# Kernel tuning notes

Hardware: AMD Instinct MI355X
Metric: run time of the kernel (lower is better)

## Reference

```python
import jax, jax.numpy as jnp
import numpy as np

EMBED = 512
HEADS = 8
HEAD_DIM = EMBED // HEADS
N, T = 512, 64


def setup_inputs() -> dict:
    key = jax.random.key(0)
    ks = jax.random.split(key, 11)
    s = 1.0 / np.sqrt(EMBED)
    inp = {
        'values': jax.random.normal(ks[0], (N, T, EMBED), jnp.float32),
        'keys':   jax.random.normal(ks[1], (N, T, EMBED), jnp.float32),
        'query':  jax.random.normal(ks[2], (N, T, EMBED), jnp.float32),
        'Wv': jax.random.uniform(ks[3], (EMBED, EMBED), jnp.float32, -s, s),
        'bv': jax.random.uniform(ks[4], (EMBED,), jnp.float32, -s, s),
        'Wk': jax.random.uniform(ks[5], (EMBED, EMBED), jnp.float32, -s, s),
        'bk': jax.random.uniform(ks[6], (EMBED,), jnp.float32, -s, s),
        'Wq': jax.random.uniform(ks[7], (EMBED, EMBED), jnp.float32, -s, s),
        'bq': jax.random.uniform(ks[8], (EMBED,), jnp.float32, -s, s),
        'Wo': jax.random.uniform(ks[9], (EMBED, EMBED), jnp.float32, -s, s),
        'bo': jax.random.uniform(ks[10], (EMBED,), jnp.float32, -s, s),
    }
    return inp


def reference(values, keys, query, Wv, bv, Wk, bk, Wq, bq, Wo, bo):
    n, t, c = query.shape
    v = (values @ Wv.T + bv).reshape(n, t, HEADS, HEAD_DIM)
    k = (keys   @ Wk.T + bk).reshape(n, t, HEADS, HEAD_DIM)
    q = (query  @ Wq.T + bq).reshape(n, t, HEADS, HEAD_DIM)
    # attention over the batch axis: energy[q,k,t,h]
    energy = jnp.einsum('qthd,kthd->qkth', q, k)
    attn = jax.nn.softmax(energy / jnp.sqrt(jnp.float32(EMBED)), axis=1)
    out = jnp.einsum('qkth,kthd->qthd', attn, v).reshape(n, t, HEADS * HEAD_DIM)
    return out @ Wo.T + bo
```

## Files before the change

kernel.cpp:

```cpp
#include <hip/hip_runtime.h>
#include <hip/hip_bf16.h>
#include <math.h>

#define NBATCH 512
#define TT 64
#define EMB 512
#define NHEADS 8
#define HDIM 64
#define MROWS (NBATCH * TT)
#define ROWSTRIDE (TT * EMB)
#define WSEG 262144

static constexpr float QSCALE = 0.0637587140f;

typedef __attribute__((ext_vector_type(8))) short short8v;
typedef __attribute__((ext_vector_type(4))) float f32x4;

__device__ __forceinline__ unsigned short f2bf(float x) {
    union { float f; unsigned int u; } v; v.f = x;
    unsigned int r = v.u + 0x7fff + ((v.u >> 16) & 1);
    return (unsigned short)(r >> 16);
}

__device__ __forceinline__ unsigned int cvtpk(float lo, float hi) {
    unsigned int r;
    asm("v_cvt_pk_bf16_f32 %0, %1, %2" : "=v"(r) : "v"(lo), "v"(hi));
    return r;
}

__device__ __forceinline__ void gl16(const void* g, void* l) {
    __builtin_amdgcn_global_load_lds(
        (const __attribute__((address_space(1))) unsigned int*)g,
        (__attribute__((address_space(3))) unsigned int*)l, 16, 0, 0);
}

__global__ __launch_bounds__(256) void cvt3(
    const float* __restrict__ a, const float* __restrict__ b, const float* __restrict__ c,
    unsigned short* __restrict__ oa, unsigned short* __restrict__ ob, unsigned short* __restrict__ oc)
{
    const size_t i = (size_t)blockIdx.x * 256 + threadIdx.x;
    float4 va = reinterpret_cast<const float4*>(a)[i];
    float4 vb = reinterpret_cast<const float4*>(b)[i];
    float4 vc = reinterpret_cast<const float4*>(c)[i];
    ushort4 ra, rb, rc;
    ra.x = f2bf(va.x); ra.y = f2bf(va.y); ra.z = f2bf(va.z); ra.w = f2bf(va.w);
    rb.x = f2bf(vb.x); rb.y = f2bf(vb.y); rb.z = f2bf(vb.z); rb.w = f2bf(vb.w);
    rc.x = f2bf(vc.x); rc.y = f2bf(vc.y); rc.z = f2bf(vc.z); rc.w = f2bf(vc.w);
    reinterpret_cast<ushort4*>(oa)[i] = ra;
    reinterpret_cast<ushort4*>(ob)[i] = rb;
    reinterpret_cast<ushort4*>(oc)[i] = rc;
}

__global__ __launch_bounds__(256) void cvtw(
    const float* __restrict__ w0, const float* __restrict__ w1,
    const float* __restrict__ w2, const float* __restrict__ w3,
    unsigned short* __restrict__ dst)
{
    const int seg = blockIdx.y;
    const float* src = (seg == 0) ? w0 : (seg == 1) ? w1 : (seg == 2) ? w2 : w3;
    const float sc = (seg == 0) ? QSCALE : 1.0f;
    const size_t i = (size_t)blockIdx.x * 256 + threadIdx.x;
    float4 v = reinterpret_cast<const float4*>(src)[i];
    ushort4 r;
    r.x = f2bf(v.x * sc); r.y = f2bf(v.y * sc); r.z = f2bf(v.z * sc); r.w = f2bf(v.w * sc);
    reinterpret_cast<ushort4*>(dst + (size_t)seg * WSEG)[i] = r;
}

__global__ __launch_bounds__(512, 2) void gemm_proj3(
    const unsigned short* __restrict__ A0, const unsigned short* __restrict__ A1,
    const unsigned short* __restrict__ A2, const unsigned short* __restrict__ Wb,
    const float* __restrict__ b0, const float* __restrict__ b1, const float* __restrict__ b2,
    unsigned short* __restrict__ o0, unsigned short* __restrict__ o1, unsigned short* __restrict__ o2)
{
    __shared__ __align__(16) unsigned short Asb[2][256 * 64];
    __shared__ __align__(16) unsigned short Bsb[2][256 * 64];
    const int z = blockIdx.z;
    const unsigned short* A = (z == 0) ? A0 : (z == 1) ? A1 : A2;
    const unsigned short* W = Wb + (size_t)z * WSEG;
    const float* bias = (z == 0) ? b0 : (z == 1) ? b1 : b2;
    const float bsc = (z == 0) ? QSCALE : 1.0f;
    unsigned short* Cout = (z == 0) ? o0 : (z == 1) ? o1 : o2;

    const int tid = threadIdx.x;
    const int wave = tid >> 6, lane = tid & 63;
    const int lg = lane >> 4, li = lane & 15;
    const int m0 = blockIdx.x * 256;
    const int n0 = blockIdx.y * 256;
    const int wm = (wave >> 2) * 128;
    const int wn = (wave & 3) * 64;

    f32x4 acc[8][4] = {};

    const int au = (tid & 7) ^ ((tid >> 3) & 7);
    const unsigned short* gA = A + (size_t)(m0 + (tid >> 3)) * 512 + au * 8;
    const unsigned short* gW = W + (size_t)(n0 + (tid >> 3)) * 512 + au * 8;

#define ISSUE(t, bb) do {                                                   \
        const int _k0 = (t) * 64;                                           \
        _Pragma("unroll")                                                   \
        for (int _i = 0; _i < 4; _i++) {                                    \
            gl16(gA + _k0 + (size_t)_i * 64 * 512,                          \
                 &Asb[bb][wave * 512 + _i * 4096]);                         \
            gl16(gW + _k0 + (size_t)_i * 64 * 512,                          \
                 &Bsb[bb][wave * 512 + _i * 4096]);                         \
        }                                                                   \
    } while (0)

    ISSUE(0, 0);
    ISSUE(1, 1);

    for (int t = 0; t < 8; ++t) {
        if (t < 7) { asm volatile("s_waitcnt vmcnt(8)" ::: "memory"); }
        else       { asm volatile("s_waitcnt vmcnt(0)" ::: "memory"); }
        __builtin_amdgcn_s_barrier();
        __builtin_amdgcn_sched_barrier(0);

        const int b = t & 1;
        __builtin_amdgcn_s_setprio(1);
#pragma unroll
        for (int kf = 0; kf < 2; kf++) {
            const int xofs = (kf * 32 + lg * 8);
            short8v bfr[4];
#pragma unroll
            for (int nf = 0; nf < 4; nf++) {
                const int rB = wn + nf * 16 + li;
                bfr[nf] = *reinterpret_cast<const short8v*>(
                    &Bsb[b][rB * 64 + (xofs ^ ((rB & 7) * 8))]);
            }
#pragma unroll
            for (int mf = 0; mf < 8; mf++) {
                const int rA = wm + mf * 16 + li;
                const short8v af = *reinterpret_cast<const short8v*>(
                    &Asb[b][rA * 64 + (xofs ^ ((rA & 7) * 8))]);
#pragma unroll
                for (int nf = 0; nf < 4; nf++)
                    acc[mf][nf] = __builtin_amdgcn_mfma_f32_16x16x32_bf16(af, bfr[nf], acc[mf][nf], 0, 0, 0);
            }
        }
        __builtin_amdgcn_s_setprio(0);

        asm volatile("s_waitcnt lgkmcnt(0)" ::: "memory");
        __builtin_amdgcn_s_barrier();
        __builtin_amdgcn_sched_barrier(0);
        if (t + 2 < 8) ISSUE(t + 2, b);
    }
#undef ISSUE

#pragma unroll
    for (int nf = 0; nf < 4; nf++) {
        const int col = n0 + wn + nf * 16 + li;
        const float bb = bias[col] * bsc;
#pragma unroll
        for (int mf = 0; mf < 8; mf++) {
            const int row0 = m0 + wm + mf * 16 + lg * 4;
#pragma unroll
            for (int r = 0; r < 4; r++)
                Cout[(size_t)(row0 + r) * 512 + col] = f2bf(acc[mf][nf][r] + bb);
        }
    }
}

__global__ __launch_bounds__(256) void gemm_out(
    const unsigned short* __restrict__ A, const unsigned short* __restrict__ W,
    const float* __restrict__ bias, float* __restrict__ Cout)
{
    __shared__ __align__(16) unsigned short As[128 * 32];
    __shared__ __align__(16) unsigned short Bs[128 * 32];
    const int tid = threadIdx.x;
    const int wave = tid >> 6, lane = tid & 63;
    const int lg = lane >> 4, li = lane & 15;
    const int m0 = blockIdx.x * 128;
    const int n0 = blockIdx.y * 128;
    const int wr = (wave >> 1) * 64;
    const int wc = (wave & 1) * 64;

    f32x4 acc[4][4] = {};

    const unsigned short* ga = A + (size_t)(m0 + (tid >> 2)) * 512 + (tid & 3) * 8;
    const unsigned short* gb = W + (size_t)(n0 + (tid >> 2)) * 512 + (tid & 3) * 8;
    unsigned short* lA = &As[wave * 512];
    unsigned short* lB = &Bs[wave * 512];

    for (int k0 = 0; k0 < 512; k0 += 32) {
        __syncthreads();
        gl16(ga + k0, lA);
        gl16(ga + k0 + 64 * 512, lA + 2048);
        gl16(gb + k0, lB);
        gl16(gb + k0 + 64 * 512, lB + 2048);
        __syncthreads();

        short8v af[4], bfr[4];
#pragma unroll
        for (int i = 0; i < 4; i++) {
            af[i]  = *reinterpret_cast<const short8v*>(&As[(wr + i * 16 + li) * 32 + lg * 8]);
            bfr[i] = *reinterpret_cast<const short8v*>(&Bs[(wc + i * 16 + li) * 32 + lg * 8]);
        }
#pragma unroll
        for (int i = 0; i < 4; i++)
#pragma unroll
            for (int j = 0; j < 4; j++)
                acc[i][j] = __builtin_amdgcn_mfma_f32_16x16x32_bf16(af[i], bfr[j], acc[i][j], 0, 0, 0);
    }

#pragma unroll
    for (int j = 0; j < 4; j++) {
        const int col = n0 + wc + j * 16 + li;
        const float bb = bias[col];
#pragma unroll
        for (int i = 0; i < 4; i++) {
            const int row0 = m0 + wr + i * 16 + lg * 4;
#pragma unroll
            for (int r = 0; r < 4; r++)
                Cout[(size_t)(row0 + r) * 512 + col] = acc[i][j][r] + bb;
        }
    }
}

__global__ __launch_bounds__(256) void attn_bf16(
    const unsigned short* __restrict__ qp, const unsigned short* __restrict__ kp,
    const unsigned short* __restrict__ vp, unsigned short* __restrict__ ao)
{
    __shared__ __align__(16) unsigned short Ks[64 * 64];
    __shared__ __align__(16) unsigned short Vt[64][68];
    __shared__ __align__(16) unsigned short Pl[4][16][72];

    const int tid = threadIdx.x;
    const int wave = tid >> 6, lane = tid & 63;
    const int lg = lane >> 4, li = lane & 15;
    const int n0 = blockIdx.x * 256;
    const int th = blockIdx.y;
    const size_t base = (size_t)(th >> 3) * EMB + (size_t)(th & 7) * HDIM;

    short8v qf[4][2];
#pragma unroll
    for (int mf = 0; mf < 4; mf++)
#pragma unroll
        for (int kf = 0; kf < 2; kf++)
            qf[mf][kf] = *reinterpret_cast<const short8v*>(
                qp + (size_t)(n0 + wave * 64 + mf * 16 + li) * ROWSTRIDE
                   + base + kf * 32 + lg * 8);

    const int vd0 = (tid & 15) * 4;
    const int vk0 = (tid >> 4) * 4;
    const unsigned short* gv = vp + base + vd0;
    uint2 vl[4];
#pragma unroll
    for (int i = 0; i < 4; i++)
        vl[i] = *reinterpret_cast<const uint2*>(gv + (size_t)(vk0 + i) * ROWSTRIDE);

    const short8v ones = (short8v)(short)0x3F80;
    f32x4 acc[4][4] = {};
    f32x4 acc_l[4] = {};

    for (int kv = 0; kv < 8; kv++) {
        const int k0 = kv * 64;
        __syncthreads();

        {
            unsigned short* lk = &Ks[wave * 512];
#pragma unroll
            for (int i = 0; i < 2; i++) {
                const int r = (tid >> 3) + i * 32;
                const int srcofs = (((tid & 7) * 8) ^ ((r & 7) * 8));
                gl16(kp + (size_t)(k0 + r) * ROWSTRIDE + base + srcofs, lk + i * 2048);
            }
        }
#pragma unroll
        for (int dd = 0; dd < 4; dd++) {
            const unsigned int sel = (dd & 1) ? 0x07060302u : 0x05040100u;
            const unsigned int a = (dd < 2) ? vl[0].x : vl[0].y;
            const unsigned int b = (dd < 2) ? vl[1].x : vl[1].y;
            const unsigned int c = (dd < 2) ? vl[2].x : vl[2].y;
            const unsigned int d = (dd < 2) ? vl[3].x : vl[3].y;
            uint2 o;
            o.x = __builtin_amdgcn_perm(b, a, sel);
            o.y = __builtin_amdgcn_perm(d, c, sel);
            *reinterpret_cast<uint2*>(&Vt[vd0 + dd][vk0]) = o;
        }
        __syncthreads();

        if (kv < 7) {
#pragma unroll
            for (int i = 0; i < 4; i++)
                vl[i] = *reinterpret_cast<const uint2*>(
                    gv + (size_t)(k0 + 64 + vk0 + i) * ROWSTRIDE);
        }

        short8v kfr[4][2], vfr[4][2];
#pragma unroll
        for (int nf = 0; nf < 4; nf++) {
            const int key = nf * 16 + li;
#pragma unroll
            for (int kf = 0; kf < 2; kf++)
                kfr[nf][kf] = *reinterpret_cast<const short8v*>(
                    &Ks[key * 64 + ((kf * 32 + lg * 8) ^ ((key & 7) * 8))]);
        }
#pragma unroll
        for (int df = 0; df < 4; df++)
#pragma unroll
            for (int kf = 0; kf < 2; kf++)
                vfr[df][kf] = *reinterpret_cast<const short8v*>(
                    &Vt[df * 16 + li][kf * 32 + lg * 8]);

#pragma unroll
        for (int mf = 0; mf < 4; mf++) {
            f32x4 s[4] = {};
#pragma unroll
            for (int nf = 0; nf < 4; nf++)
#pragma unroll
                for (int kf = 0; kf < 2; kf++)
                    s[nf] = __builtin_amdgcn_mfma_f32_16x16x32_bf16(kfr[nf][kf], qf[mf][kf], s[nf], 0, 0, 0);

#pragma unroll
            for (int nf = 0; nf < 4; nf++) {
                const float p0 = exp2f(s[nf][0]);
                const float p1 = exp2f(s[nf][1]);
                const float p2 = exp2f(s[nf][2]);
                const float p3 = exp2f(s[nf][3]);
                union { unsigned int u[2]; uint2 v; } pk2;
                pk2.u[0] = cvtpk(p0, p1);
                pk2.u[1] = cvtpk(p2, p3);
                *reinterpret_cast<uint2*>(&Pl[wave][li][nf * 16 + lg * 4]) = pk2.v;
            }

            short8v pf[2];
#pragma unroll
            for (int kf = 0; kf < 2; kf++)
                pf[kf] = *reinterpret_cast<const short8v*>(
                    &Pl[wave][li][kf * 32 + lg * 8]);
#pragma unroll
            for (int kf = 0; kf < 2; kf++)
                acc_l[mf] = __builtin_amdgcn_mfma_f32_16x16x32_bf16(pf[kf], ones, acc_l[mf], 0, 0, 0);
#pragma unroll
            for (int df = 0; df < 4; df++)
#pragma unroll
                for (int kf = 0; kf < 2; kf++)
                    acc[mf][df] = __builtin_amdgcn_mfma_f32_16x16x32_bf16(pf[kf], vfr[df][kf], acc[mf][df], 0, 0, 0);
        }
    }

#pragma unroll
    for (int mf = 0; mf < 4; mf++) {
#pragma unroll
        for (int r = 0; r < 4; r++) {
            const float linv = 1.0f / acc_l[mf][r];
            const int qrow = n0 + wave * 64 + mf * 16 + lg * 4 + r;
#pragma unroll
            for (int df = 0; df < 4; df++)
                ao[(size_t)qrow * ROWSTRIDE + base + df * 16 + li] = f2bf(acc[mf][df][r] * linv);
        }
    }
}

extern "C" void kernel_launch(void* const* d_in, const int* in_sizes, int n_in,
                              void* d_out, int out_size, void* d_ws, size_t ws_size,
                              hipStream_t stream) {
    const float* values = (const float*)d_in[0];
    const float* keys   = (const float*)d_in[1];
    const float* query  = (const float*)d_in[2];
    const float* Wv = (const float*)d_in[3];
    const float* bv = (const float*)d_in[4];
    const float* Wk = (const float*)d_in[5];
    const float* bk = (const float*)d_in[6];
    const float* Wq = (const float*)d_in[7];
    const float* bq = (const float*)d_in[8];
    const float* Wo = (const float*)d_in[9];
    const float* bo = (const float*)d_in[10];
    float* out = (float*)d_out;

    unsigned short* ws16 = (unsigned short*)d_ws;
    const size_t PLANE = (size_t)MROWS * EMB;
    unsigned short* xq = ws16;
    unsigned short* xk = ws16 + PLANE;
    unsigned short* xv = ws16 + 2 * PLANE;
    unsigned short* qb = ws16 + 3 * PLANE;
    unsigned short* kb = ws16 + 4 * PLANE;
    unsigned short* vb = ws16 + 5 * PLANE;
    unsigned short* ab = ws16 + 6 * PLANE;
    unsigned short* wb = ws16 + 7 * PLANE;

    cvt3<<<PLANE / 4 / 256, 256, 0, stream>>>(query, keys, values, xq, xk, xv);
    cvtw<<<dim3(WSEG / 4 / 256, 4), 256, 0, stream>>>(Wq, Wk, Wv, Wo, wb);

    gemm_proj3<<<dim3(MROWS / 256, EMB / 256, 3), 512, 0, stream>>>(
        xq, xk, xv, wb, bq, bk, bv, qb, kb, vb);

    attn_bf16<<<dim3(2, TT * NHEADS), 256, 0, stream>>>(qb, kb, vb, ab);

    gemm_out<<<dim3(MROWS / 128, EMB / 128), 256, 0, stream>>>(
        ab, wb + 3 * WSEG, bo, out);
}
```

Baseline: 244.0 us.

## Fuse fp32-to-bf16 input conversion into projection GEMM A-tile loading

Removes the separate cvt3 kernel, which read the three fp32 activation planes and wrote bf16 copies. The projection GEMM now loads fp32 A tiles into registers, converts them with packed bf16 instructions, and writes them into swizzled LDS, while weights still use direct global-to-LDS loads. This saves one full write and re-read of the bf16 activations plus a kernel launch. In exchange the GEMM reads twice as many A bytes, uses more registers (the occupancy hint of 2 in launch bounds is dropped), and adds register staging and extra waits to the pipeline.

Result: faster. 220.6 us (-9.6%).

```diff
diff --git a/kernel.cpp b/kernel.cpp
--- a/kernel.cpp
+++ b/kernel.cpp
@@ -32,23 +32,6 @@
     __builtin_amdgcn_global_load_lds(
         (const __attribute__((address_space(1))) unsigned int*)g,
         (__attribute__((address_space(3))) unsigned int*)l, 16, 0, 0);
-}
-
-__global__ __launch_bounds__(256) void cvt3(
-    const float* __restrict__ a, const float* __restrict__ b, const float* __restrict__ c,
-    unsigned short* __restrict__ oa, unsigned short* __restrict__ ob, unsigned short* __restrict__ oc)
-{
-    const size_t i = (size_t)blockIdx.x * 256 + threadIdx.x;
-    float4 va = reinterpret_cast<const float4*>(a)[i];
-    float4 vb = reinterpret_cast<const float4*>(b)[i];
-    float4 vc = reinterpret_cast<const float4*>(c)[i];
-    ushort4 ra, rb, rc;
-    ra.x = f2bf(va.x); ra.y = f2bf(va.y); ra.z = f2bf(va.z); ra.w = f2bf(va.w);
-    rb.x = f2bf(vb.x); rb.y = f2bf(vb.y); rb.z = f2bf(vb.z); rb.w = f2bf(vb.w);
-    rc.x = f2bf(vc.x); rc.y = f2bf(vc.y); rc.z = f2bf(vc.z); rc.w = f2bf(vc.w);
-    reinterpret_cast<ushort4*>(oa)[i] = ra;
-    reinterpret_cast<ushort4*>(ob)[i] = rb;
-    reinterpret_cast<ushort4*>(oc)[i] = rc;
 }
 
 __global__ __launch_bounds__(256) void cvtw(
@@ -66,16 +49,16 @@
     reinterpret_cast<ushort4*>(dst + (size_t)seg * WSEG)[i] = r;
 }
 
-__global__ __launch_bounds__(512, 2) void gemm_proj3(
-    const unsigned short* __restrict__ A0, const unsigned short* __restrict__ A1,
-    const unsigned short* __restrict__ A2, const unsigned short* __restrict__ Wb,
+__global__ __launch_bounds__(512) void gemm_proj3(
+    const float* __restrict__ A0, const float* __restrict__ A1,
+    const float* __restrict__ A2, const unsigned short* __restrict__ Wb,
     const float* __restrict__ b0, const float* __restrict__ b1, const float* __restrict__ b2,
     unsigned short* __restrict__ o0, unsigned short* __restrict__ o1, unsigned short* __restrict__ o2)
 {
     __shared__ __align__(16) unsigned short Asb[2][256 * 64];
     __shared__ __align__(16) unsigned short Bsb[2][256 * 64];
     const int z = blockIdx.z;
-    const unsigned short* A = (z == 0) ? A0 : (z == 1) ? A1 : A2;
+    const float* A = (z == 0) ? A0 : (z == 1) ? A1 : A2;
     const unsigned short* W = Wb + (size_t)z * WSEG;
     const float* bias = (z == 0) ? b0 : (z == 1) ? b1 : b2;
     const float bsc = (z == 0) ? QSCALE : 1.0f;
@@ -92,26 +75,54 @@
     f32x4 acc[8][4] = {};
 
     const int au = (tid & 7) ^ ((tid >> 3) & 7);
-    const unsigned short* gA = A + (size_t)(m0 + (tid >> 3)) * 512 + au * 8;
     const unsigned short* gW = W + (size_t)(n0 + (tid >> 3)) * 512 + au * 8;
-
-#define ISSUE(t, bb) do {                                                   \
+    const float* gA = A + (size_t)(m0 + (tid >> 3)) * 512 + (tid & 7) * 8;
+    const int arow = tid >> 3;
+    const int apo = ((tid & 7) ^ (arow & 7)) * 8;
+
+    float4 rA[8];
+
+#define LOADA(t) do {                                                       \
         const int _k0 = (t) * 64;                                           \
         _Pragma("unroll")                                                   \
         for (int _i = 0; _i < 4; _i++) {                                    \
-            gl16(gA + _k0 + (size_t)_i * 64 * 512,                          \
-                 &Asb[bb][wave * 512 + _i * 4096]);                         \
+            rA[2 * _i]     = *reinterpret_cast<const float4*>(gA + _k0 + (size_t)_i * 64 * 512);     \
+            rA[2 * _i + 1] = *reinterpret_cast<const float4*>(gA + _k0 + (size_t)_i * 64 * 512 + 4); \
+        }                                                                   \
+    } while (0)
+
+#define ISSUEW(t, bb) do {                                                  \
+        const int _k0 = (t) * 64;                                           \
+        _Pragma("unroll")                                                   \
+        for (int _i = 0; _i < 4; _i++)                                      \
             gl16(gW + _k0 + (size_t)_i * 64 * 512,                          \
                  &Bsb[bb][wave * 512 + _i * 4096]);                         \
+    } while (0)
+
+#define WRITEA(bb) do {                                                     \
+        _Pragma("unroll")                                                   \
+        for (int _i = 0; _i < 4; _i++) {                                    \
+            union { unsigned int u[4]; short8v v; } _pk;                    \
+            _pk.u[0] = cvtpk(rA[2 * _i].x, rA[2 * _i].y);                   \
+            _pk.u[1] = cvtpk(rA[2 * _i].z, rA[2 * _i].w);                   \
+            _pk.u[2] = cvtpk(rA[2 * _i + 1].x, rA[2 * _i + 1].y);           \
+            _pk.u[3] = cvtpk(rA[2 * _i + 1].z, rA[2 * _i + 1].w);           \
+            *reinterpret_cast<short8v*>(                                    \
+                &Asb[bb][(size_t)(arow + _i * 64) * 64 + apo]) = _pk.v;     \
         }                                                                   \
     } while (0)
 
-    ISSUE(0, 0);
-    ISSUE(1, 1);
+    LOADA(0);
+    ISSUEW(0, 0);
+    asm volatile("s_waitcnt vmcnt(4)" ::: "memory");
+    WRITEA(0);
+    LOADA(1);
+    ISSUEW(1, 1);
 
     for (int t = 0; t < 8; ++t) {
-        if (t < 7) { asm volatile("s_waitcnt vmcnt(8)" ::: "memory"); }
+        if (t < 7) { asm volatile("s_waitcnt vmcnt(12)" ::: "memory"); }
         else       { asm volatile("s_waitcnt vmcnt(0)" ::: "memory"); }
+        asm volatile("s_waitcnt lgkmcnt(0)" ::: "memory");
         __builtin_amdgcn_s_barrier();
         __builtin_amdgcn_sched_barrier(0);
 
@@ -129,9 +140,9 @@
             }
 #pragma unroll
             for (int mf = 0; mf < 8; mf++) {
-                const int rA = wm + mf * 16 + li;
+                const int rA_ = wm + mf * 16 + li;
                 const short8v af = *reinterpret_cast<const short8v*>(
-                    &Asb[b][rA * 64 + (xofs ^ ((rA & 7) * 8))]);
+                    &Asb[b][rA_ * 64 + (xofs ^ ((rA_ & 7) * 8))]);
 #pragma unroll
                 for (int nf = 0; nf < 4; nf++)
                     acc[mf][nf] = __builtin_amdgcn_mfma_f32_16x16x32_bf16(af, bfr[nf], acc[mf][nf], 0, 0, 0);
@@ -142,9 +153,19 @@
         asm volatile("s_waitcnt lgkmcnt(0)" ::: "memory");
         __builtin_amdgcn_s_barrier();
         __builtin_amdgcn_sched_barrier(0);
-        if (t + 2 < 8) ISSUE(t + 2, b);
-    }
-#undef ISSUE
+
+        if (t + 1 < 8) {
+            asm volatile("s_waitcnt vmcnt(4)" ::: "memory");
+            WRITEA((t + 1) & 1);
+            if (t + 2 < 8) {
+                LOADA(t + 2);
+                ISSUEW(t + 2, b);
+            }
+        }
+    }
+#undef LOADA
+#undef ISSUEW
+#undef WRITEA
 
 #pragma unroll
     for (int nf = 0; nf < 4; nf++) {
@@ -370,20 +391,16 @@
 
     unsigned short* ws16 = (unsigned short*)d_ws;
     const size_t PLANE = (size_t)MROWS * EMB;
-    unsigned short* xq = ws16;
-    unsigned short* xk = ws16 + PLANE;
-    unsigned short* xv = ws16 + 2 * PLANE;
-    unsigned short* qb = ws16 + 3 * PLANE;
-    unsigned short* kb = ws16 + 4 * PLANE;
-    unsigned short* vb = ws16 + 5 * PLANE;
-    unsigned short* ab = ws16 + 6 * PLANE;
-    unsigned short* wb = ws16 + 7 * PLANE;
-
-    cvt3<<<PLANE / 4 / 256, 256, 0, stream>>>(query, keys, values, xq, xk, xv);
+    unsigned short* qb = ws16;
+    unsigned short* kb = ws16 + PLANE;
+    unsigned short* vb = ws16 + 2 * PLANE;
+    unsigned short* ab = ws16 + 3 * PLANE;
+    unsigned short* wb = ws16 + 4 * PLANE;
+
     cvtw<<<dim3(WSEG / 4 / 256, 4), 256, 0, stream>>>(Wq, Wk, Wv, Wo, wb);
 
     gemm_proj3<<<dim3(MROWS / 256, EMB / 256, 3), 512, 0, stream>>>(
-        xq, xk, xv, wb, bq, bk, bv, qb, kb, vb);
+        query, keys, values, wb, bq, bk, bv, qb, kb, vb);
 
     attn_bf16<<<dim3(2, TT * NHEADS), 256, 0, stream>>>(qb, kb, vb, ab);
 
```
